# Performance work log

Measured on AMD Instinct MI355X. Metric: run time of the kernel, lower is better.

## Reference

```python
import jax, jax.numpy as jnp
import numpy as np

TOP_K = 2  # matches init_kwargs k

def setup_inputs() -> dict:
    key = jax.random.key(0)
    k1, k2 = jax.random.split(key)
    x = jax.random.normal(k1, (4, 4096, 2048), dtype=jnp.float32)
    gate_w = jax.random.normal(k2, (8, 2048), dtype=jnp.float32) * 0.02  # Linear weight [E, D]
    return {"x": x, "gate_w": gate_w}

def reference(x, gate_w):
    B, S, D = x.shape
    E = gate_w.shape[0]
    xf = x.reshape(-1, D)                              # [N, D], N = B*S
    gate_logits = jnp.einsum('nd,ed->ne', xf, gate_w)  # [N, E]
    probs = jax.nn.softmax(gate_logits.astype(jnp.float32), axis=-1)
    weights, selected = jax.lax.top_k(probs, TOP_K)    # [N, K], [N, K]
    weights = weights / jnp.sum(weights, axis=-1, keepdims=True)
    weights = weights.astype(x.dtype)
    # one_hot -> [N, K, E], permute(2,1,0) -> [E, K, N]
    expert_mask = jax.nn.one_hot(selected, E, dtype=jnp.int32).transpose(2, 1, 0)
    return weights, expert_mask, gate_logits
```

## Files before the change

kernel.cpp:

```cpp
#include <hip/hip_runtime.h>
#include <math.h>


constexpr int kN = 16384;
constexpr int kD = 2048;
constexpr int kE = 8;

using f4 = __attribute__((ext_vector_type(4))) float;

__global__ __launch_bounds__(256, 4)
void moe_router_kernel(const float* __restrict__ x,
                       const float* __restrict__ gw,
                       float* __restrict__ out)
{
    const int lane = threadIdx.x & 63;
    const int wv   = threadIdx.x >> 6;
    const int n0   = blockIdx.x * 16 + wv * 4;

    const float* xr = x + (long)n0 * kD;

    float acc[4][8];
#pragma unroll
    for (int r = 0; r < 4; ++r)
#pragma unroll
        for (int e = 0; e < 8; ++e) acc[r][e] = 0.f;

#pragma unroll 1
    for (int it = 0; it < 8; ++it) {
        const int c = it * 256 + lane * 4;
        f4 xv[4];
#pragma unroll
        for (int r = 0; r < 4; ++r)
            xv[r] = __builtin_nontemporal_load(
                reinterpret_cast<const f4*>(xr + (long)r * kD + c));
        f4 g[8];
#pragma unroll
        for (int e = 0; e < 8; ++e)
            g[e] = *reinterpret_cast<const f4*>(gw + e * kD + c);
#pragma unroll
        for (int r = 0; r < 4; ++r)
#pragma unroll
            for (int e = 0; e < 8; ++e) {
                acc[r][e] = fmaf(xv[r].x, g[e].x, acc[r][e]);
                acc[r][e] = fmaf(xv[r].y, g[e].y, acc[r][e]);
                acc[r][e] = fmaf(xv[r].z, g[e].z, acc[r][e]);
                acc[r][e] = fmaf(xv[r].w, g[e].w, acc[r][e]);
            }
    }

    const int rsel = lane & 1;
    float a2[2][8];
#pragma unroll
    for (int j = 0; j < 2; ++j)
#pragma unroll
        for (int e = 0; e < 8; ++e) {
            const float mine  = rsel ? acc[2 * j + 1][e] : acc[2 * j][e];
            const float other = rsel ? acc[2 * j][e]     : acc[2 * j + 1][e];
            a2[j][e] = mine + __shfl_xor(other, 1);
        }
    const int sel = (lane >> 1) & 1;
    float a1[8];
#pragma unroll
    for (int e = 0; e < 8; ++e) {
        const float mine  = sel ? a2[1][e] : a2[0][e];
        const float other = sel ? a2[0][e] : a2[1][e];
        a1[e] = mine + __shfl_xor(other, 2);
    }
#pragma unroll
    for (int e = 0; e < 8; ++e) {
        float v = a1[e];
        v += __shfl_xor(v, 4);
        v += __shfl_xor(v, 8);
        v += __shfl_xor(v, 16);
        v += __shfl_xor(v, 32);
        a1[e] = v;
    }

    int s0 = 0; float b0 = a1[0];
#pragma unroll
    for (int e = 1; e < 8; ++e)
        if (a1[e] > b0) { b0 = a1[e]; s0 = e; }
    int s1 = 0; float b1 = -3.4e38f;
#pragma unroll
    for (int e = 0; e < 8; ++e) {
        const bool t = (e != s0) && (a1[e] > b1);
        b1 = t ? a1[e] : b1;
        s1 = t ? e : s1;
    }
    const float d  = expf(b1 - b0);
    const float w0 = 1.0f / (1.0f + d);
    const float w1 = d * w0;

    float* out_w = out;
    float* out_m = out + 2 * kN;
    float* out_l = out + 2 * kN + 2 * kE * kN;

    const int row = lane & 3;
    const int q   = lane >> 2;

    {
        const int em = lane >> 3;
        const int km = (lane >> 2) & 1;
        const int ss = km ? s1 : s0;
        out_m[(long)em * (2 * kN) + (long)km * kN + (n0 + row)] =
            (ss == em) ? 1.0f : 0.0f;
    }
    if (lane < 8)
        out_w[(long)(n0 + row) * 2 + q] = q ? w1 : w0;
    if (lane < 32) {
        float v = a1[0];
#pragma unroll
        for (int e = 1; e < 8; ++e)
            v = (q == e) ? a1[e] : v;
        out_l[(long)(n0 + row) * 8 + q] = v;
    }
}

extern "C" void kernel_launch(void* const* d_in, const int* in_sizes, int n_in,
                              void* d_out, int out_size, void* d_ws, size_t ws_size,
                              hipStream_t stream)
{
    (void)in_sizes; (void)n_in; (void)d_ws; (void)ws_size; (void)out_size;
    const float* x  = (const float*)d_in[0];
    const float* gw = (const float*)d_in[1];
    float* out = (float*)d_out;

    dim3 grid(kN / 16);
    dim3 block(256);
    moe_router_kernel<<<grid, block, 0, stream>>>(x, gw, out);
}
```

Baseline: 32.65 us.

## Stage gate weights in LDS and double-buffer x loads with larger blocks

Each block copies the full gate weight matrix into shared memory once and reads it from LDS in the inner loop instead of from global memory. The x row loads for the next iteration are issued before computing the current one, to overlap memory latency with FMAs. Blocks grow to 512 threads covering 32 rows, and the expert loop is split in halves to limit live registers. The 64 KB LDS footprint and per-block fill add startup cost and cap resident blocks per CU.

```diff
diff --git a/kernel.cpp b/kernel.cpp
--- a/kernel.cpp
+++ b/kernel.cpp
@@ -8,14 +8,24 @@
 
 using f4 = __attribute__((ext_vector_type(4))) float;
 
-__global__ __launch_bounds__(256, 4)
+__global__ __launch_bounds__(512, 4)
 void moe_router_kernel(const float* __restrict__ x,
                        const float* __restrict__ gw,
                        float* __restrict__ out)
 {
-    const int lane = threadIdx.x & 63;
-    const int wv   = threadIdx.x >> 6;
-    const int n0   = blockIdx.x * 16 + wv * 4;
+    __shared__ float sg[kE * kD];
+
+    const int tid  = threadIdx.x;
+    const int lane = tid & 63;
+    const int wv   = tid >> 6;
+    const int n0   = blockIdx.x * 32 + wv * 4;
+
+#pragma unroll
+    for (int j = 0; j < 8; ++j) {
+        const int idx = (j * 512 + tid) * 4;
+        *reinterpret_cast<f4*>(sg + idx) = *reinterpret_cast<const f4*>(gw + idx);
+    }
+    __syncthreads();
 
     const float* xr = x + (long)n0 * kD;
 
@@ -25,27 +35,49 @@
 #pragma unroll
         for (int e = 0; e < 8; ++e) acc[r][e] = 0.f;
 
+    f4 xv[4], xn[4];
+#pragma unroll
+    for (int r = 0; r < 4; ++r)
+        xv[r] = __builtin_nontemporal_load(
+            reinterpret_cast<const f4*>(xr + (long)r * kD + lane * 4));
+
 #pragma unroll 1
     for (int it = 0; it < 8; ++it) {
+        if (it < 7) {
+            const int cn = (it + 1) * 256 + lane * 4;
+#pragma unroll
+            for (int r = 0; r < 4; ++r)
+                xn[r] = __builtin_nontemporal_load(
+                    reinterpret_cast<const f4*>(xr + (long)r * kD + cn));
+        }
         const int c = it * 256 + lane * 4;
-        f4 xv[4];
+        f4 g[4];
 #pragma unroll
-        for (int r = 0; r < 4; ++r)
-            xv[r] = __builtin_nontemporal_load(
-                reinterpret_cast<const f4*>(xr + (long)r * kD + c));
-        f4 g[8];
-#pragma unroll
-        for (int e = 0; e < 8; ++e)
-            g[e] = *reinterpret_cast<const f4*>(gw + e * kD + c);
+        for (int e = 0; e < 4; ++e)
+            g[e] = *reinterpret_cast<const f4*>(sg + e * kD + c);
 #pragma unroll
         for (int r = 0; r < 4; ++r)
 #pragma unroll
-            for (int e = 0; e < 8; ++e) {
+            for (int e = 0; e < 4; ++e) {
                 acc[r][e] = fmaf(xv[r].x, g[e].x, acc[r][e]);
                 acc[r][e] = fmaf(xv[r].y, g[e].y, acc[r][e]);
                 acc[r][e] = fmaf(xv[r].z, g[e].z, acc[r][e]);
                 acc[r][e] = fmaf(xv[r].w, g[e].w, acc[r][e]);
             }
+#pragma unroll
+        for (int e = 0; e < 4; ++e)
+            g[e] = *reinterpret_cast<const f4*>(sg + (e + 4) * kD + c);
+#pragma unroll
+        for (int r = 0; r < 4; ++r)
+#pragma unroll
+            for (int e = 0; e < 4; ++e) {
+                acc[r][e + 4] = fmaf(xv[r].x, g[e].x, acc[r][e + 4]);
+                acc[r][e + 4] = fmaf(xv[r].y, g[e].y, acc[r][e + 4]);
+                acc[r][e + 4] = fmaf(xv[r].z, g[e].z, acc[r][e + 4]);
+                acc[r][e + 4] = fmaf(xv[r].w, g[e].w, acc[r][e + 4]);
+            }
+#pragma unroll
+        for (int r = 0; r < 4; ++r) xv[r] = xn[r];
     }
 
     const int rsel = lane & 1;
@@ -125,7 +157,7 @@
     const float* gw = (const float*)d_in[1];
     float* out = (float*)d_out;
 
-    dim3 grid(kN / 16);
-    dim3 block(256);
+    dim3 grid(kN / 32);
+    dim3 block(512);
     moe_router_kernel<<<grid, block, 0, stream>>>(x, gw, out);
 }
```

Result: slower. 39.08 us (+19.7%).

## Split D across waves with register-resident gate weights and LDS cross-wave reduction

Applied to the files above, without the earlier changes.

Each block now handles 32 rows with 512 threads. Every wave owns a fixed 256-column slice of D, and its gate weights are loaded into registers once. Rows stream through a 4-deep software prefetch ring of nontemporal loads, and per-wave partial logits are reduced across waves through double-buffered LDS and a barrier. This removes the repeated gate-weight reloads and keeps more loads in flight, at the cost of a block barrier per 8-row group and serializing the top-k/output work onto one wave per group.

```diff
diff --git a/kernel.cpp b/kernel.cpp
--- a/kernel.cpp
+++ b/kernel.cpp
@@ -8,111 +8,134 @@
 
 using f4 = __attribute__((ext_vector_type(4))) float;
 
-__global__ __launch_bounds__(256, 4)
+__global__ __launch_bounds__(512, 4)
 void moe_router_kernel(const float* __restrict__ x,
                        const float* __restrict__ gw,
                        float* __restrict__ out)
 {
-    const int lane = threadIdx.x & 63;
-    const int wv   = threadIdx.x >> 6;
-    const int n0   = blockIdx.x * 16 + wv * 4;
+    __shared__ float part[2][512];
 
-    const float* xr = x + (long)n0 * kD;
+    const int tid  = threadIdx.x;
+    const int lane = tid & 63;
+    const int wv   = tid >> 6;
+    const int col  = wv * 256 + lane * 4;
+    const int rowbase = blockIdx.x * 32;
 
-    float acc[4][8];
+    const float* xc = x + col;
+
+    f4 g[8];
 #pragma unroll
-    for (int r = 0; r < 4; ++r)
-#pragma unroll
-        for (int e = 0; e < 8; ++e) acc[r][e] = 0.f;
-
-#pragma unroll 1
-    for (int it = 0; it < 8; ++it) {
-        const int c = it * 256 + lane * 4;
-        f4 xv[4];
-#pragma unroll
-        for (int r = 0; r < 4; ++r)
-            xv[r] = __builtin_nontemporal_load(
-                reinterpret_cast<const f4*>(xr + (long)r * kD + c));
-        f4 g[8];
-#pragma unroll
-        for (int e = 0; e < 8; ++e)
-            g[e] = *reinterpret_cast<const f4*>(gw + e * kD + c);
-#pragma unroll
-        for (int r = 0; r < 4; ++r)
-#pragma unroll
-            for (int e = 0; e < 8; ++e) {
-                acc[r][e] = fmaf(xv[r].x, g[e].x, acc[r][e]);
-                acc[r][e] = fmaf(xv[r].y, g[e].y, acc[r][e]);
-                acc[r][e] = fmaf(xv[r].z, g[e].z, acc[r][e]);
-                acc[r][e] = fmaf(xv[r].w, g[e].w, acc[r][e]);
-            }
-    }
-
-    const int rsel = lane & 1;
-    float a2[2][8];
-#pragma unroll
-    for (int j = 0; j < 2; ++j)
-#pragma unroll
-        for (int e = 0; e < 8; ++e) {
-            const float mine  = rsel ? acc[2 * j + 1][e] : acc[2 * j][e];
-            const float other = rsel ? acc[2 * j][e]     : acc[2 * j + 1][e];
-            a2[j][e] = mine + __shfl_xor(other, 1);
-        }
-    const int sel = (lane >> 1) & 1;
-    float a1[8];
-#pragma unroll
-    for (int e = 0; e < 8; ++e) {
-        const float mine  = sel ? a2[1][e] : a2[0][e];
-        const float other = sel ? a2[0][e] : a2[1][e];
-        a1[e] = mine + __shfl_xor(other, 2);
-    }
-#pragma unroll
-    for (int e = 0; e < 8; ++e) {
-        float v = a1[e];
-        v += __shfl_xor(v, 4);
-        v += __shfl_xor(v, 8);
-        v += __shfl_xor(v, 16);
-        v += __shfl_xor(v, 32);
-        a1[e] = v;
-    }
-
-    int s0 = 0; float b0 = a1[0];
-#pragma unroll
-    for (int e = 1; e < 8; ++e)
-        if (a1[e] > b0) { b0 = a1[e]; s0 = e; }
-    int s1 = 0; float b1 = -3.4e38f;
-#pragma unroll
-    for (int e = 0; e < 8; ++e) {
-        const bool t = (e != s0) && (a1[e] > b1);
-        b1 = t ? a1[e] : b1;
-        s1 = t ? e : s1;
-    }
-    const float d  = expf(b1 - b0);
-    const float w0 = 1.0f / (1.0f + d);
-    const float w1 = d * w0;
+    for (int e = 0; e < 8; ++e)
+        g[e] = *reinterpret_cast<const f4*>(gw + e * kD + col);
 
     float* out_w = out;
     float* out_m = out + 2 * kN;
     float* out_l = out + 2 * kN + 2 * kE * kN;
 
-    const int row = lane & 3;
-    const int q   = lane >> 2;
+    f4 xb[4];
+#pragma unroll
+    for (int p = 0; p < 3; ++p)
+        xb[p] = __builtin_nontemporal_load(
+            reinterpret_cast<const f4*>(xc + (long)(rowbase + p) * kD));
 
-    {
-        const int em = lane >> 3;
-        const int km = (lane >> 2) & 1;
-        const int ss = km ? s1 : s0;
-        out_m[(long)em * (2 * kN) + (long)km * kN + (n0 + row)] =
-            (ss == em) ? 1.0f : 0.0f;
-    }
-    if (lane < 8)
-        out_w[(long)(n0 + row) * 2 + q] = q ? w1 : w0;
-    if (lane < 32) {
-        float v = a1[0];
+    float acc[8][8];
+    const int b0 = lane & 1, b1 = (lane >> 1) & 1, b2 = (lane >> 2) & 1;
+
+#pragma unroll 1
+    for (int gidx = 0; gidx < 4; ++gidx) {
+        const int r0 = rowbase + gidx * 8;
+
 #pragma unroll
-        for (int e = 1; e < 8; ++e)
-            v = (q == e) ? a1[e] : v;
-        out_l[(long)(n0 + row) * 8 + q] = v;
+        for (int r = 0; r < 8; ++r) {
+            int prow = r0 + r + 3;
+            prow = prow > kN - 1 ? kN - 1 : prow;
+            xb[(r + 3) & 3] = __builtin_nontemporal_load(
+                reinterpret_cast<const f4*>(xc + (long)prow * kD));
+            const f4 xv = xb[r & 3];
+#pragma unroll
+            for (int e = 0; e < 8; ++e) {
+                float t = xv.x * g[e].x;
+                t = fmaf(xv.y, g[e].y, t);
+                t = fmaf(xv.z, g[e].z, t);
+                acc[r][e] = fmaf(xv.w, g[e].w, t);
+            }
+        }
+
+#pragma unroll
+        for (int j = 0; j < 4; ++j)
+#pragma unroll
+            for (int e = 0; e < 8; ++e) {
+                const float mine  = b0 ? acc[2 * j + 1][e] : acc[2 * j][e];
+                const float other = b0 ? acc[2 * j][e]     : acc[2 * j + 1][e];
+                acc[j][e] = mine + __shfl_xor(other, 1);
+            }
+#pragma unroll
+        for (int k = 0; k < 2; ++k)
+#pragma unroll
+            for (int e = 0; e < 8; ++e) {
+                const float mine  = b1 ? acc[2 * k + 1][e] : acc[2 * k][e];
+                const float other = b1 ? acc[2 * k][e]     : acc[2 * k + 1][e];
+                acc[k][e] = mine + __shfl_xor(other, 2);
+            }
+#pragma unroll
+        for (int e = 0; e < 8; ++e) {
+            const float mine  = b2 ? acc[1][e] : acc[0][e];
+            const float other = b2 ? acc[0][e] : acc[1][e];
+            float v = mine + __shfl_xor(other, 4);
+            v += __shfl_xor(v, 8);
+            v += __shfl_xor(v, 16);
+            v += __shfl_xor(v, 32);
+            acc[0][e] = v;
+        }
+
+        {
+            const int er = lane >> 3;
+            float v = acc[0][0];
+#pragma unroll
+            for (int e = 1; e < 8; ++e) v = (er == e) ? acc[0][e] : v;
+            part[gidx & 1][wv * 64 + (lane & 7) * 8 + er] = v;
+        }
+        asm volatile("s_waitcnt lgkmcnt(0)" ::: "memory");
+        __builtin_amdgcn_sched_barrier(0);
+        __builtin_amdgcn_s_barrier();
+        __builtin_amdgcn_sched_barrier(0);
+
+        if (wv == gidx) {
+            const int r = lane & 7, c = lane >> 3;
+            const float* pb = &part[gidx & 1][0];
+            float L = 0.f;
+#pragma unroll
+            for (int w = 0; w < 8; ++w)
+                L += pb[w * 64 + r * 8 + c];
+
+            float le[8];
+#pragma unroll
+            for (int e = 0; e < 8; ++e)
+                le[e] = __shfl(L, r + 8 * e);
+
+            int s0 = 0; float v0 = le[0];
+#pragma unroll
+            for (int e = 1; e < 8; ++e)
+                if (le[e] > v0) { v0 = le[e]; s0 = e; }
+            int s1 = 0; float v1 = -3.4e38f;
+#pragma unroll
+            for (int e = 0; e < 8; ++e) {
+                const bool t = (e != s0) && (le[e] > v1);
+                v1 = t ? le[e] : v1;
+                s1 = t ? e : s1;
+            }
+            const float d  = expf(v1 - v0);
+            const float w0 = 1.0f / (1.0f + d);
+            const float w1 = d * w0;
+
+            out_l[(long)(r0 + r) * 8 + c] = L;
+            out_m[(long)c * (2 * kN) + (r0 + r)]      = (s0 == c) ? 1.0f : 0.0f;
+            out_m[(long)c * (2 * kN) + kN + (r0 + r)] = (s1 == c) ? 1.0f : 0.0f;
+            if (c == 0) {
+                float2 wp; wp.x = w0; wp.y = w1;
+                *reinterpret_cast<float2*>(out_w + (long)(r0 + r) * 2) = wp;
+            }
+        }
     }
 }
 
@@ -125,7 +148,7 @@
     const float* gw = (const float*)d_in[1];
     float* out = (float*)d_out;
 
-    dim3 grid(kN / 16);
-    dim3 block(256);
+    dim3 grid(kN / 32);
+    dim3 block(512);
     moe_router_kernel<<<grid, block, 0, stream>>>(x, gw, out);
 }
```

Measured after the change: 30.45 us. 1.07x faster.

## Process two rows per wave with split gate loads to raise occupancy

Applied to the files above, without the earlier changes.

Each wave now handles 2 rows instead of 4, so the grid doubles and launch bounds ask for 8 blocks per CU. Gate weights are loaded in two halves of 4 experts to cut register pressure, and the shuffle reduction and output indexing are adjusted to match. The nontemporal hint on x loads is dropped. Each gate-weight load is now reused across fewer rows, so more redundant cache traffic on gw is traded for more waves to hide memory latency.

```diff
diff --git a/kernel.cpp b/kernel.cpp
--- a/kernel.cpp
+++ b/kernel.cpp
@@ -8,67 +8,74 @@
 
 using f4 = __attribute__((ext_vector_type(4))) float;
 
-__global__ __launch_bounds__(256, 4)
+__global__ __launch_bounds__(256, 8)
 void moe_router_kernel(const float* __restrict__ x,
                        const float* __restrict__ gw,
                        float* __restrict__ out)
 {
     const int lane = threadIdx.x & 63;
     const int wv   = threadIdx.x >> 6;
-    const int n0   = blockIdx.x * 16 + wv * 4;
+    const int n0   = blockIdx.x * 8 + wv * 2;
 
     const float* xr = x + (long)n0 * kD;
 
-    float acc[4][8];
+    float acc0[8], acc1[8];
 #pragma unroll
-    for (int r = 0; r < 4; ++r)
-#pragma unroll
-        for (int e = 0; e < 8; ++e) acc[r][e] = 0.f;
+    for (int e = 0; e < 8; ++e) { acc0[e] = 0.f; acc1[e] = 0.f; }
 
 #pragma unroll 1
     for (int it = 0; it < 8; ++it) {
         const int c = it * 256 + lane * 4;
-        f4 xv[4];
+        const f4 xv0 = *reinterpret_cast<const f4*>(xr + c);
+        const f4 xv1 = *reinterpret_cast<const f4*>(xr + kD + c);
+        {
+            f4 g[4];
 #pragma unroll
-        for (int r = 0; r < 4; ++r)
-            xv[r] = __builtin_nontemporal_load(
-                reinterpret_cast<const f4*>(xr + (long)r * kD + c));
-        f4 g[8];
+            for (int e = 0; e < 4; ++e)
+                g[e] = *reinterpret_cast<const f4*>(gw + e * kD + c);
 #pragma unroll
-        for (int e = 0; e < 8; ++e)
-            g[e] = *reinterpret_cast<const f4*>(gw + e * kD + c);
+            for (int e = 0; e < 4; ++e) {
+                float t0 = fmaf(xv0.x, g[e].x, acc0[e]);
+                t0 = fmaf(xv0.y, g[e].y, t0);
+                t0 = fmaf(xv0.z, g[e].z, t0);
+                acc0[e] = fmaf(xv0.w, g[e].w, t0);
+                float t1 = fmaf(xv1.x, g[e].x, acc1[e]);
+                t1 = fmaf(xv1.y, g[e].y, t1);
+                t1 = fmaf(xv1.z, g[e].z, t1);
+                acc1[e] = fmaf(xv1.w, g[e].w, t1);
+            }
+        }
+        {
+            f4 g[4];
 #pragma unroll
-        for (int r = 0; r < 4; ++r)
+            for (int e = 0; e < 4; ++e)
+                g[e] = *reinterpret_cast<const f4*>(gw + (e + 4) * kD + c);
 #pragma unroll
-            for (int e = 0; e < 8; ++e) {
-                acc[r][e] = fmaf(xv[r].x, g[e].x, acc[r][e]);
-                acc[r][e] = fmaf(xv[r].y, g[e].y, acc[r][e]);
-                acc[r][e] = fmaf(xv[r].z, g[e].z, acc[r][e]);
-                acc[r][e] = fmaf(xv[r].w, g[e].w, acc[r][e]);
+            for (int e = 0; e < 4; ++e) {
+                float t0 = fmaf(xv0.x, g[e].x, acc0[e + 4]);
+                t0 = fmaf(xv0.y, g[e].y, t0);
+                t0 = fmaf(xv0.z, g[e].z, t0);
+                acc0[e + 4] = fmaf(xv0.w, g[e].w, t0);
+                float t1 = fmaf(xv1.x, g[e].x, acc1[e + 4]);
+                t1 = fmaf(xv1.y, g[e].y, t1);
+                t1 = fmaf(xv1.z, g[e].z, t1);
+                acc1[e + 4] = fmaf(xv1.w, g[e].w, t1);
             }
+        }
     }
 
-    const int rsel = lane & 1;
-    float a2[2][8];
-#pragma unroll
-    for (int j = 0; j < 2; ++j)
-#pragma unroll
-        for (int e = 0; e < 8; ++e) {
-            const float mine  = rsel ? acc[2 * j + 1][e] : acc[2 * j][e];
-            const float other = rsel ? acc[2 * j][e]     : acc[2 * j + 1][e];
-            a2[j][e] = mine + __shfl_xor(other, 1);
-        }
-    const int sel = (lane >> 1) & 1;
+    const int rp = lane & 1;
     float a1[8];
 #pragma unroll
     for (int e = 0; e < 8; ++e) {
-        const float mine  = sel ? a2[1][e] : a2[0][e];
-        const float other = sel ? a2[0][e] : a2[1][e];
-        a1[e] = mine + __shfl_xor(other, 2);
+        const float mine  = rp ? acc1[e] : acc0[e];
+        const float other = rp ? acc0[e] : acc1[e];
+        a1[e] = mine + __shfl_xor(other, 1);
     }
 #pragma unroll
     for (int e = 0; e < 8; ++e) {
         float v = a1[e];
+        v += __shfl_xor(v, 2);
         v += __shfl_xor(v, 4);
         v += __shfl_xor(v, 8);
         v += __shfl_xor(v, 16);
@@ -95,24 +102,24 @@
     float* out_m = out + 2 * kN;
     float* out_l = out + 2 * kN + 2 * kE * kN;
 
-    const int row = lane & 3;
-    const int q   = lane >> 2;
+    const int row = lane & 1;
 
-    {
-        const int em = lane >> 3;
-        const int km = (lane >> 2) & 1;
+    if (lane < 32) {
+        const int em = lane >> 2;
+        const int km = (lane >> 1) & 1;
         const int ss = km ? s1 : s0;
         out_m[(long)em * (2 * kN) + (long)km * kN + (n0 + row)] =
             (ss == em) ? 1.0f : 0.0f;
     }
-    if (lane < 8)
-        out_w[(long)(n0 + row) * 2 + q] = q ? w1 : w0;
-    if (lane < 32) {
+    if (lane < 4)
+        out_w[(long)(n0 + row) * 2 + (lane >> 1)] = (lane >> 1) ? w1 : w0;
+    if (lane < 16) {
+        const int el = lane >> 1;
         float v = a1[0];
 #pragma unroll
         for (int e = 1; e < 8; ++e)
-            v = (q == e) ? a1[e] : v;
-        out_l[(long)(n0 + row) * 8 + q] = v;
+            v = (el == e) ? a1[e] : v;
+        out_l[(long)(n0 + row) * 8 + el] = v;
     }
 }
 
@@ -125,7 +132,7 @@
     const float* gw = (const float*)d_in[1];
     float* out = (float*)d_out;
 
-    dim3 grid(kN / 16);
+    dim3 grid(kN / 8);
     dim3 block(256);
     moe_router_kernel<<<grid, block, 0, stream>>>(x, gw, out);
 }
```

After: 33.43 us. +2.4%, slower.
